# Kernel tuning notes

Hardware: AMD Instinct MI355X
Metric: run time of the kernel (lower is better)

The kernel has to match this reference:

```python
import jax, jax.numpy as jnp
import numpy as np
from jax import lax

EPS_W = 1e-8
EPS_BN = 1e-5
MLP = (256, 256, 128)
IN_C = 384


def setup_inputs() -> dict:
    key = jax.random.key(0)
    ks = jax.random.split(key, 20)
    B, N, M, C1, C2 = 4, 16384, 4096, 128, 256
    inp = {
        'xyz1': jax.random.normal(ks[0], (B, N, 3), jnp.float32),
        'xyz2': jax.random.normal(ks[1], (B, M, 3), jnp.float32),
        'pts1': jax.random.normal(ks[2], (B, N, C1), jnp.float32),
        'pts2': jax.random.normal(ks[3], (B, M, C2), jnp.float32),
    }
    c_in = IN_C
    for li, c_out in enumerate(MLP):
        scale = 1.0 / np.sqrt(c_in)
        inp[f'w{li}'] = jax.random.uniform(ks[4 + 4 * li], (c_out, c_in), jnp.float32, -scale, scale)
        inp[f'b{li}'] = jax.random.uniform(ks[5 + 4 * li], (c_out,), jnp.float32, -scale, scale)
        inp[f'g{li}'] = jnp.ones((c_out,), jnp.float32)   # BN gamma
        inp[f'be{li}'] = jnp.zeros((c_out,), jnp.float32)  # BN beta
        c_in = c_out
    return inp


def _fp_forward(xyz1, xyz2, pts1, pts2, params):
    B, N, _ = xyz1.shape
    M = xyz2.shape[1]
    # squared pairwise distances [B, N, M] (three_nn returns squared dists)
    d2 = (jnp.sum(xyz1 * xyz1, -1)[:, :, None]
          + jnp.sum(xyz2 * xyz2, -1)[:, None, :]
          - 2.0 * jnp.einsum('bnd,bmd->bnm', xyz1, xyz2))
    neg_d, idx = lax.top_k(-d2, 3)          # 3 nearest neighbors
    d = -neg_d                               # [B, N, 3]
    w = 1.0 / (d + EPS_W)
    w = w / jnp.sum(w, axis=2, keepdims=True)
    # gather neighbor features: pts2 [B, M, C2], idx [B, N, 3]
    C2 = pts2.shape[-1]
    gathered = jnp.take_along_axis(pts2, idx.reshape(B, N * 3)[..., None], axis=1)
    gathered = gathered.reshape(B, N, 3, C2)
    interp = jnp.einsum('bnkc,bnk->bnc', gathered, w)
    x = jnp.concatenate([pts1, interp], axis=-1)  # [B, N, in_c]
    for (wl, bl, gl, bel) in params:
        h = jnp.einsum('bnc,oc->bno', x, wl) + bl      # conv1x1
        mean = jnp.mean(h, axis=(0, 1))                # BN over (B, N), training stats
        var = jnp.mean((h - mean) ** 2, axis=(0, 1))   # biased variance (torch BN)
        h = (h - mean) * lax.rsqrt(var + EPS_BN) * gl + bel
        x = jax.nn.relu(h)
    return x


def reference(xyz1, xyz2, pts1, pts2,
              w0, b0, g0, be0, w1, b1, g1, be1, w2, b2, g2, be2):
    params = [(w0, b0, g0, be0), (w1, b1, g1, be1), (w2, b2, g2, be2)]
    return _fp_forward(xyz1, xyz2, pts1, pts2, params)
```

## Files before the change

kernel.cpp:

```cpp
#include <hip/hip_runtime.h>
#include <hip/hip_fp16.h>
#include <stdint.h>

typedef _Float16 f16;
typedef _Float16 f16x8 __attribute__((ext_vector_type(8)));
typedef _Float16 f16x4 __attribute__((ext_vector_type(4)));
typedef _Float16 f16x2 __attribute__((ext_vector_type(2)));
typedef float f32x4 __attribute__((ext_vector_type(4)));
typedef float f32x2 __attribute__((ext_vector_type(2)));

#define B_ 4
#define N_ 16384
#define M_ 4096
#define C1_ 128
#define C2_ 256
#define BNTOT 65536

#define SPLIT 16
#define CHUNK (M_ / SPLIT)
#define QPT 2

__device__ __forceinline__ void gload_lds16(const void* g, void* l) {
    __builtin_amdgcn_global_load_lds(
        (const __attribute__((address_space(1))) void*)g,
        (__attribute__((address_space(3))) void*)l, 16, 0, 0);
}

#define NN_INSERT(k0, k1, k2, i0, i1, i2, d2, mi)                          \
    if (d2 < k2) {                                                         \
        if (d2 < k1) {                                                     \
            k2 = k1; i2 = i1;                                              \
            if (d2 < k0) { k1 = k0; i1 = i0; k0 = d2; i0 = mi; }           \
            else         { k1 = d2; i1 = mi; }                             \
        } else { k2 = d2; i2 = mi; }                                       \
    }

__global__ void conv_f16_kernel(const float* __restrict__ s0, f16* __restrict__ d0,
                                const float* __restrict__ s1, f16* __restrict__ d1,
                                const float* __restrict__ s2, f16* __restrict__ d2,
                                float* __restrict__ statz) {
    int i = blockIdx.x * blockDim.x + threadIdx.x;
    if (i < 98304) d0[i] = (f16)s0[i];
    if (i < 65536) d1[i] = (f16)s1[i];
    if (i < 32768) d2[i] = (f16)s2[i];
    if (i < 1536) statz[i] = 0.0f;
}

__global__ __launch_bounds__(256) void nn_part_kernel(
    const float* __restrict__ xyz1, const float* __restrict__ xyz2,
    f32x2* __restrict__ ck) {
    __shared__ __align__(16) float xs[CHUNK];
    __shared__ __align__(16) float ys[CHUNK];
    __shared__ __align__(16) float zs[CHUNK];
    int bid = blockIdx.x;
    int part = bid & (SPLIT - 1);
    int pblk = bid >> 4;
    int b = pblk >> 5;
    int m0 = part * CHUNK;
    const float* x2 = xyz2 + ((size_t)b * M_ + m0) * 3;
    {
        int m = threadIdx.x;
        xs[m] = x2[m * 3 + 0];
        ys[m] = x2[m * 3 + 1];
        zs[m] = x2[m * 3 + 2];
    }
    __syncthreads();
    size_t p0 = (size_t)pblk * 512 + threadIdx.x;
    const float* q0p = xyz1 + p0 * 3;
    const float* q1p = xyz1 + (p0 + 256) * 3;
    float q0x = q0p[0], q0y = q0p[1], q0z = q0p[2];
    float q1x = q1p[0], q1y = q1p[1], q1z = q1p[2];
    float a0 = 3.4e38f, a1 = 3.4e38f, a2 = 3.4e38f;
    float b0 = 3.4e38f, b1 = 3.4e38f, b2 = 3.4e38f;
    int ai0 = 0, ai1 = 0, ai2 = 0;
    int bi0 = 0, bi1 = 0, bi2 = 0;
    for (int m = 0; m < CHUNK; m += 4) {
        f32x4 xv = *(const f32x4*)&xs[m];
        f32x4 yv = *(const f32x4*)&ys[m];
        f32x4 zv = *(const f32x4*)&zs[m];
#pragma unroll
        for (int u = 0; u < 4; ++u) {
            float cx = xv[u], cy = yv[u], cz = zv[u];
            int mi = m0 + m + u;
            {
                float dx = q0x - cx, dy = q0y - cy, dz = q0z - cz;
                float d2 = fmaf(dx, dx, fmaf(dy, dy, dz * dz));
                NN_INSERT(a0, a1, a2, ai0, ai1, ai2, d2, mi)
            }
            {
                float dx = q1x - cx, dy = q1y - cy, dz = q1z - cz;
                float d2 = fmaf(dx, dx, fmaf(dy, dy, dz * dz));
                NN_INSERT(b0, b1, b2, bi0, bi1, bi2, d2, mi)
            }
        }
    }
    f32x2 e;
    e[0] = a0; e[1] = __int_as_float(ai0);
    __builtin_nontemporal_store(e, ck + (size_t)(0 * SPLIT + part) * BNTOT + p0);
    e[0] = a1; e[1] = __int_as_float(ai1);
    __builtin_nontemporal_store(e, ck + (size_t)(1 * SPLIT + part) * BNTOT + p0);
    e[0] = a2; e[1] = __int_as_float(ai2);
    __builtin_nontemporal_store(e, ck + (size_t)(2 * SPLIT + part) * BNTOT + p0);
    e[0] = b0; e[1] = __int_as_float(bi0);
    __builtin_nontemporal_store(e, ck + (size_t)(0 * SPLIT + part) * BNTOT + p0 + 256);
    e[0] = b1; e[1] = __int_as_float(bi1);
    __builtin_nontemporal_store(e, ck + (size_t)(1 * SPLIT + part) * BNTOT + p0 + 256);
    e[0] = b2; e[1] = __int_as_float(bi2);
    __builtin_nontemporal_store(e, ck + (size_t)(2 * SPLIT + part) * BNTOT + p0 + 256);
}

__global__ __launch_bounds__(256) void nn_merge_kernel(
    const f32x2* __restrict__ ck,
    int* __restrict__ idx_out, float* __restrict__ w_out) {
    size_t p = (size_t)blockIdx.x * 256 + threadIdx.x;
    float k0 = 3.4e38f, k1 = 3.4e38f, k2 = 3.4e38f;
    int i0 = 0, i1 = 0, i2 = 0;
#pragma unroll
    for (int part = 0; part < SPLIT; ++part) {
#pragma unroll
        for (int rank = 0; rank < 3; ++rank) {
            f32x2 e = __builtin_nontemporal_load(ck + (size_t)(rank * SPLIT + part) * BNTOT + p);
            float x = e[0];
            int ix = __float_as_int(e[1]);
            bool c0 = x < k0, c1 = x < k1, c2 = x < k2;
            float mx = c0 ? k0 : x;  int mxi = c0 ? i0 : ix;
            float m2 = c1 ? k1 : x;  int m2i = c1 ? i1 : ix;
            k0 = c0 ? x : k0;   i0 = c0 ? ix : i0;
            k1 = c1 ? mx : k1;  i1 = c1 ? mxi : i1;
            k2 = c2 ? m2 : k2;  i2 = c2 ? m2i : i2;
        }
    }
    float w0 = 1.0f / (k0 + 1e-8f);
    float w1 = 1.0f / (k1 + 1e-8f);
    float w2 = 1.0f / (k2 + 1e-8f);
    float ws = w0 + w1 + w2;
    w0 /= ws; w1 /= ws; w2 /= ws;
    idx_out[p * 3 + 0] = i0; idx_out[p * 3 + 1] = i1; idx_out[p * 3 + 2] = i2;
    w_out[p * 3 + 0] = w0;  w_out[p * 3 + 1] = w1;  w_out[p * 3 + 2] = w2;
}

__global__ __launch_bounds__(256) void interp_kernel(
    const float* __restrict__ pts1, const float* __restrict__ pts2,
    const int* __restrict__ idxb, const float* __restrict__ wb,
    f16* __restrict__ x0) {
    int wave = threadIdx.x >> 6, lane = threadIdx.x & 63;
    size_t p = (size_t)blockIdx.x * 4 + wave;
    int batch = (int)(p >> 14);
    int j0 = idxb[p * 3 + 0], j1 = idxb[p * 3 + 1], j2 = idxb[p * 3 + 2];
    float w0 = wb[p * 3 + 0], w1 = wb[p * 3 + 1], w2 = wb[p * 3 + 2];
    const float* base2 = pts2 + (size_t)batch * M_ * C2_;
    f32x4 a = *(const f32x4*)(base2 + (size_t)j0 * C2_ + lane * 4);
    f32x4 bv = *(const f32x4*)(base2 + (size_t)j1 * C2_ + lane * 4);
    f32x4 c = *(const f32x4*)(base2 + (size_t)j2 * C2_ + lane * 4);
    f16* xrow = x0 + p * (C1_ + C2_);
    f16x4 o;
#pragma unroll
    for (int j = 0; j < 4; ++j)
        o[j] = (f16)(w0 * a[j] + w1 * bv[j] + w2 * c[j]);
    __builtin_nontemporal_store(o, (f16x4*)(xrow + C1_ + lane * 4));
    f32x2 p1 = __builtin_nontemporal_load((const f32x2*)(pts1 + p * C1_ + lane * 2));
    f16x2 o2; o2[0] = (f16)p1[0]; o2[1] = (f16)p1[1];
    __builtin_nontemporal_store(o2, (f16x2*)(xrow + lane * 2));
}

template <int K>
__global__ __launch_bounds__(256) void gemm_f16(
    const f16* __restrict__ A, const f16* __restrict__ W,
    f16* __restrict__ H, float* __restrict__ sums, float* __restrict__ sumsq,
    int Nn) {
    __shared__ __align__(16) f16 As[128 * 64];
    __shared__ __align__(16) f16 Bs[128 * 64];
    int tid = threadIdx.x;
    int lane = tid & 63, wave = tid >> 6;
    int wr = wave >> 1, wc = wave & 1;
    int bm0 = blockIdx.x * 128, bn0 = blockIdx.y * 128;
    const f16* Ab = A + (size_t)bm0 * K;
    const f16* Wb = W + (size_t)bn0 * K;
    int r = tid >> 3;
    int cc = (tid & 7) * 8;
    f32x4 acc[4][4] = {};
    for (int kt = 0; kt < K; kt += 64) {
        __syncthreads();
#pragma unroll
        for (int i = 0; i < 4; ++i) {
            gload_lds16(Ab + (size_t)(i * 32 + r) * K + kt + cc, &As[(i * 32 + r) * 64 + cc]);
            gload_lds16(Wb + (size_t)(i * 32 + r) * K + kt + cc, &Bs[(i * 32 + r) * 64 + cc]);
        }
        __syncthreads();
#pragma unroll
        for (int kk = 0; kk < 2; ++kk) {
            f16x8 af[4], bf[4];
            int koff = kk * 32 + (lane >> 4) * 8;
#pragma unroll
            for (int mt = 0; mt < 4; ++mt)
                af[mt] = *(const f16x8*)&As[(wr * 64 + mt * 16 + (lane & 15)) * 64 + koff];
#pragma unroll
            for (int nt = 0; nt < 4; ++nt)
                bf[nt] = *(const f16x8*)&Bs[(wc * 64 + nt * 16 + (lane & 15)) * 64 + koff];
#pragma unroll
            for (int mt = 0; mt < 4; ++mt)
#pragma unroll
                for (int nt = 0; nt < 4; ++nt)
                    acc[mt][nt] = __builtin_amdgcn_mfma_f32_16x16x32_f16(af[mt], bf[nt], acc[mt][nt], 0, 0, 0);
        }
    }
    int rr = (lane >> 4) * 4;
    int cl = lane & 15;
#pragma unroll
    for (int mt = 0; mt < 4; ++mt) {
#pragma unroll
        for (int nt = 0; nt < 4; ++nt) {
            int row = bm0 + wr * 64 + mt * 16 + rr;
            int col = bn0 + wc * 64 + nt * 16 + cl;
#pragma unroll
            for (int j = 0; j < 4; ++j)
                H[(size_t)(row + j) * Nn + col] = (f16)acc[mt][nt][j];
        }
    }
#pragma unroll
    for (int nt = 0; nt < 4; ++nt) {
        float s = 0.f, s2 = 0.f;
#pragma unroll
        for (int mt = 0; mt < 4; ++mt)
#pragma unroll
            for (int j = 0; j < 4; ++j) {
                float v = acc[mt][nt][j];
                s += v;
                s2 = fmaf(v, v, s2);
            }
        s += __shfl_xor(s, 16);
        s2 += __shfl_xor(s2, 16);
        s += __shfl_xor(s, 32);
        s2 += __shfl_xor(s2, 32);
        if (lane < 16) {
            int c = bn0 + wc * 64 + nt * 16 + lane;
            atomicAdd(&sums[c], s);
            atomicAdd(&sumsq[c], s2);
        }
    }
}

template <bool OUT16>
__global__ __launch_bounds__(256) void bnrelu_kernel(
    const f16* __restrict__ H, const float* __restrict__ sums, const float* __restrict__ sumsq,
    const float* __restrict__ g, const float* __restrict__ be,
    f16* __restrict__ o16, float* __restrict__ o32, int Nn) {
    __shared__ float ssc[256], ssh[256];
    int tid = threadIdx.x;
    if (tid < Nn) {
        const float invM = 1.0f / 65536.0f;
        float mean = sums[tid] * invM;
        float var = sumsq[tid] * invM - mean * mean;
        float rstd = rsqrtf(var + 1e-5f);
        float sc = rstd * g[tid];
        ssc[tid] = sc;
        ssh[tid] = be[tid] - mean * sc;
    }
    __syncthreads();
    size_t t = (size_t)blockIdx.x * 256 + tid;
    size_t base = t * 8;
    int c0 = (int)(base & (size_t)(Nn - 1));
    f16x8 v = *(const f16x8*)(H + base);
    float r[8];
#pragma unroll
    for (int j = 0; j < 8; ++j)
        r[j] = fmaxf(0.0f, fmaf((float)v[j], ssc[c0 + j], ssh[c0 + j]));
    if (OUT16) {
        f16x8 ov;
#pragma unroll
        for (int j = 0; j < 8; ++j) ov[j] = (f16)r[j];
        *(f16x8*)(o16 + base) = ov;
    } else {
        f32x4 a = {r[0], r[1], r[2], r[3]};
        f32x4 b = {r[4], r[5], r[6], r[7]};
        __builtin_nontemporal_store(a, (f32x4*)(o32 + base));
        __builtin_nontemporal_store(b, (f32x4*)(o32 + base + 4));
    }
}

extern "C" void kernel_launch(void* const* d_in, const int* in_sizes, int n_in,
                              void* d_out, int out_size, void* d_ws, size_t ws_size,
                              hipStream_t stream) {
    const float* xyz1 = (const float*)d_in[0];
    const float* xyz2 = (const float*)d_in[1];
    const float* pts1 = (const float*)d_in[2];
    const float* pts2 = (const float*)d_in[3];
    const float* w0f = (const float*)d_in[4];
    const float* g0 = (const float*)d_in[6];
    const float* be0 = (const float*)d_in[7];
    const float* w1f = (const float*)d_in[8];
    const float* g1 = (const float*)d_in[10];
    const float* be1 = (const float*)d_in[11];
    const float* w2f = (const float*)d_in[12];
    const float* g2 = (const float*)d_in[14];
    const float* be2 = (const float*)d_in[15];

    char* ws = (char*)d_ws;
    f16* x0 = (f16*)(ws + 0);
    f16* bufA = (f16*)(ws + 50331648);
    f16* bufB = x0;
    f32x2* ck = (f32x2*)(ws + 50331648);
    f16* wb0 = (f16*)(ws + 83886080);
    f16* wb1 = wb0 + 98304;
    f16* wb2 = wb1 + 65536;
    int* idxb = (int*)(ws + 84279296);
    float* wgt = (float*)(ws + 85065728);
    float* stats = (float*)(ws + 85852160);
    float* sums0 = stats,        *sumsq0 = stats + 256;
    float* sums1 = stats + 512,  *sumsq1 = stats + 768;
    float* sums2 = stats + 1024, *sumsq2 = stats + 1280;

    conv_f16_kernel<<<384, 256, 0, stream>>>(w0f, wb0, w1f, wb1, w2f, wb2, stats);

    nn_part_kernel<<<(BNTOT / (256 * QPT)) * SPLIT, 256, 0, stream>>>(xyz1, xyz2, ck);
    nn_merge_kernel<<<BNTOT / 256, 256, 0, stream>>>(ck, idxb, wgt);
    interp_kernel<<<BNTOT / 4, 256, 0, stream>>>(pts1, pts2, idxb, wgt, x0);

    gemm_f16<384><<<dim3(512, 2), 256, 0, stream>>>(x0, wb0, bufA, sums0, sumsq0, 256);
    bnrelu_kernel<true><<<8192, 256, 0, stream>>>(bufA, sums0, sumsq0, g0, be0, bufA, nullptr, 256);

    gemm_f16<256><<<dim3(512, 2), 256, 0, stream>>>(bufA, wb1, bufB, sums1, sumsq1, 256);
    bnrelu_kernel<true><<<8192, 256, 0, stream>>>(bufB, sums1, sumsq1, g1, be1, bufB, nullptr, 256);

    gemm_f16<256><<<dim3(512, 1), 256, 0, stream>>>(bufB, wb2, bufA, sums2, sumsq2, 128);
    bnrelu_kernel<false><<<4096, 256, 0, stream>>>(bufA, sums2, sumsq2, g2, be2, nullptr, (float*)d_out, 128);
}
```

Measured before the change: 424.3 us.

## Fuse BN+ReLU of previous layer into next GEMM's A-tile load

```diff
diff --git a/kernel.cpp b/kernel.cpp
--- a/kernel.cpp
+++ b/kernel.cpp
@@ -240,11 +240,107 @@
     }
 }
 
-template <bool OUT16>
-__global__ __launch_bounds__(256) void bnrelu_kernel(
+__global__ __launch_bounds__(256) void gemm_bn_f16(
+    const f16* __restrict__ A, const float* __restrict__ psums,
+    const float* __restrict__ psumsq, const float* __restrict__ pg,
+    const float* __restrict__ pbe,
+    const f16* __restrict__ W, f16* __restrict__ H,
+    float* __restrict__ sums, float* __restrict__ sumsq, int Nn) {
+    const int K = 256;
+    __shared__ __align__(16) f16 As[128 * 64];
+    __shared__ __align__(16) f16 Bs[128 * 64];
+    __shared__ float ssc[K], ssh[K];
+    int tid = threadIdx.x;
+    {
+        const float invM = 1.0f / 65536.0f;
+        float mean = psums[tid] * invM;
+        float var = psumsq[tid] * invM - mean * mean;
+        float rstd = rsqrtf(var + 1e-5f);
+        float sc = rstd * pg[tid];
+        ssc[tid] = sc;
+        ssh[tid] = pbe[tid] - mean * sc;
+    }
+    int lane = tid & 63, wave = tid >> 6;
+    int wr = wave >> 1, wc = wave & 1;
+    int bm0 = blockIdx.x * 128, bn0 = blockIdx.y * 128;
+    const f16* Ab = A + (size_t)bm0 * K;
+    const f16* Wb = W + (size_t)bn0 * K;
+    int r = tid >> 3;
+    int cc = (tid & 7) * 8;
+    f32x4 acc[4][4] = {};
+    __syncthreads();
+    for (int kt = 0; kt < K; kt += 64) {
+        __syncthreads();
+#pragma unroll
+        for (int i = 0; i < 4; ++i)
+            gload_lds16(Wb + (size_t)(i * 32 + r) * K + kt + cc, &Bs[(i * 32 + r) * 64 + cc]);
+#pragma unroll
+        for (int i = 0; i < 4; ++i) {
+            f16x8 v = *(const f16x8*)(Ab + (size_t)(i * 32 + r) * K + kt + cc);
+            f16x8 o;
+#pragma unroll
+            for (int j = 0; j < 8; ++j)
+                o[j] = (f16)fmaxf(0.0f, fmaf((float)v[j], ssc[kt + cc + j], ssh[kt + cc + j]));
+            *(f16x8*)&As[(i * 32 + r) * 64 + cc] = o;
+        }
+        __syncthreads();
+#pragma unroll
+        for (int kk = 0; kk < 2; ++kk) {
+            f16x8 af[4], bf[4];
+            int koff = kk * 32 + (lane >> 4) * 8;
+#pragma unroll
+            for (int mt = 0; mt < 4; ++mt)
+                af[mt] = *(const f16x8*)&As[(wr * 64 + mt * 16 + (lane & 15)) * 64 + koff];
+#pragma unroll
+            for (int nt = 0; nt < 4; ++nt)
+                bf[nt] = *(const f16x8*)&Bs[(wc * 64 + nt * 16 + (lane & 15)) * 64 + koff];
+#pragma unroll
+            for (int mt = 0; mt < 4; ++mt)
+#pragma unroll
+                for (int nt = 0; nt < 4; ++nt)
+                    acc[mt][nt] = __builtin_amdgcn_mfma_f32_16x16x32_f16(af[mt], bf[nt], acc[mt][nt], 0, 0, 0);
+        }
+    }
+    int rr = (lane >> 4) * 4;
+    int cl = lane & 15;
+#pragma unroll
+    for (int mt = 0; mt < 4; ++mt) {
+#pragma unroll
+        for (int nt = 0; nt < 4; ++nt) {
+            int row = bm0 + wr * 64 + mt * 16 + rr;
+            int col = bn0 + wc * 64 + nt * 16 + cl;
+#pragma unroll
+            for (int j = 0; j < 4; ++j)
+                H[(size_t)(row + j) * Nn + col] = (f16)acc[mt][nt][j];
+        }
+    }
+#pragma unroll
+    for (int nt = 0; nt < 4; ++nt) {
+        float s = 0.f, s2 = 0.f;
+#pragma unroll
+        for (int mt = 0; mt < 4; ++mt)
+#pragma unroll
+            for (int j = 0; j < 4; ++j) {
+                float v = acc[mt][nt][j];
+                s += v;
+                s2 = fmaf(v, v, s2);
+            }
+        s += __shfl_xor(s, 16);
+        s2 += __shfl_xor(s2, 16);
+        s += __shfl_xor(s, 32);
+        s2 += __shfl_xor(s2, 32);
+        if (lane < 16) {
+            int c = bn0 + wc * 64 + nt * 16 + lane;
+            atomicAdd(&sums[c], s);
+            atomicAdd(&sumsq[c], s2);
+        }
+    }
+}
+
+__global__ __launch_bounds__(256) void bnrelu_f32_kernel(
     const f16* __restrict__ H, const float* __restrict__ sums, const float* __restrict__ sumsq,
     const float* __restrict__ g, const float* __restrict__ be,
-    f16* __restrict__ o16, float* __restrict__ o32, int Nn) {
+    float* __restrict__ o32, int Nn) {
     __shared__ float ssc[256], ssh[256];
     int tid = threadIdx.x;
     if (tid < Nn) {
@@ -265,17 +361,10 @@
 #pragma unroll
     for (int j = 0; j < 8; ++j)
         r[j] = fmaxf(0.0f, fmaf((float)v[j], ssc[c0 + j], ssh[c0 + j]));
-    if (OUT16) {
-        f16x8 ov;
-#pragma unroll
-        for (int j = 0; j < 8; ++j) ov[j] = (f16)r[j];
-        *(f16x8*)(o16 + base) = ov;
-    } else {
-        f32x4 a = {r[0], r[1], r[2], r[3]};
-        f32x4 b = {r[4], r[5], r[6], r[7]};
-        __builtin_nontemporal_store(a, (f32x4*)(o32 + base));
-        __builtin_nontemporal_store(b, (f32x4*)(o32 + base + 4));
-    }
+    f32x4 a = {r[0], r[1], r[2], r[3]};
+    f32x4 b = {r[4], r[5], r[6], r[7]};
+    __builtin_nontemporal_store(a, (f32x4*)(o32 + base));
+    __builtin_nontemporal_store(b, (f32x4*)(o32 + base + 4));
 }
 
 extern "C" void kernel_launch(void* const* d_in, const int* in_sizes, int n_in,
@@ -317,11 +406,13 @@
     interp_kernel<<<BNTOT / 4, 256, 0, stream>>>(pts1, pts2, idxb, wgt, x0);
 
     gemm_f16<384><<<dim3(512, 2), 256, 0, stream>>>(x0, wb0, bufA, sums0, sumsq0, 256);
-    bnrelu_kernel<true><<<8192, 256, 0, stream>>>(bufA, sums0, sumsq0, g0, be0, bufA, nullptr, 256);
-
-    gemm_f16<256><<<dim3(512, 2), 256, 0, stream>>>(bufA, wb1, bufB, sums1, sumsq1, 256);
-    bnrelu_kernel<true><<<8192, 256, 0, stream>>>(bufB, sums1, sumsq1, g1, be1, bufB, nullptr, 256);
-
-    gemm_f16<256><<<dim3(512, 1), 256, 0, stream>>>(bufB, wb2, bufA, sums2, sumsq2, 128);
-    bnrelu_kernel<false><<<4096, 256, 0, stream>>>(bufA, sums2, sumsq2, g2, be2, nullptr, (float*)d_out, 128);
-}
+
+    gemm_bn_f16<<<dim3(512, 2), 256, 0, stream>>>(bufA, sums0, sumsq0, g0, be0,
+                                                  wb1, bufB, sums1, sumsq1, 256);
+
+    gemm_bn_f16<<<dim3(512, 1), 256, 0, stream>>>(bufB, sums1, sumsq1, g1, be1,
+                                                  wb2, bufA, sums2, sumsq2, 128);
+
+    bnrelu_f32_kernel<<<4096, 256, 0, stream>>>(bufA, sums2, sumsq2, g2, be2,
+                                                (float*)d_out, 128);
+}
```

New measurement: 403.2 us. 1.05x faster.
